# Performance work log

Hardware: AMD Instinct MI355X
Metric: run time of the kernel (lower is better)

## Reference

```python
import jax, jax.numpy as jnp
import numpy as np

MODEL_DIM = 1024
TOTAL_DIM = 1024
N_HEADS = 16
HEAD_DIM = TOTAL_DIM // N_HEADS


def setup_inputs() -> dict:
    key = jax.random.key(0)
    k1, k2, k3 = jax.random.split(key, 3)
    query = jax.random.normal(k1, (2, 2048, MODEL_DIM), dtype=jnp.float32)
    # nn.Linear(model_dim, 3*total_dim, bias=False): store as [in, out] for x @ W
    W_in = jax.random.normal(k2, (MODEL_DIM, 3 * TOTAL_DIM), dtype=jnp.float32) / np.sqrt(MODEL_DIM)
    W_out = jax.random.normal(k3, (TOTAL_DIM, MODEL_DIM), dtype=jnp.float32) / np.sqrt(TOTAL_DIM)
    return {"query": query, "W_in": W_in, "W_out": W_out}


def reference(query, W_in, W_out):
    B, S, _ = query.shape
    qkv = query @ W_in                      # [B, S, 3*D]
    q, k, v = jnp.split(qkv, 3, axis=-1)    # each [B, S, D]

    def to_heads(t):
        return t.reshape(B, S, N_HEADS, HEAD_DIM).transpose(0, 2, 1, 3)  # [B,H,S,d]

    q, k, v = to_heads(q), to_heads(k), to_heads(v)
    scale = 1.0 / np.sqrt(HEAD_DIM).astype(np.float32)
    scores = jnp.einsum('bhqd,bhkd->bhqk', q, k) * scale  # [B,H,S,S]
    causal = jnp.tril(jnp.ones((S, S), dtype=bool))
    scores = jnp.where(causal, scores, jnp.finfo(scores.dtype).min)
    probs = jax.nn.softmax(scores, axis=-1)
    attn = jnp.einsum('bhqk,bhkd->bhqd', probs, v)        # [B,H,S,d]
    attn = attn.transpose(0, 2, 1, 3).reshape(B, S, TOTAL_DIM)
    return attn @ W_out                     # [B, S, model_dim]
```

## Files before the change

### kernel.cpp

```cpp
#include <hip/hip_runtime.h>


typedef __bf16 bf16x8 __attribute__((ext_vector_type(8)));
typedef float f32x4 __attribute__((ext_vector_type(4)));
typedef int i32x4 __attribute__((ext_vector_type(4)));

#define B_   2
#define S_   2048
#define DM   1024
#define NH   16
#define HD   64
#define N3   3072
#define M_   4096

#define SCALE_LOG2E 0.180336884f

__device__ __forceinline__ unsigned short f2bf(float f) {
  unsigned int u = __float_as_uint(f);
  u += 0x7fffu + ((u >> 16) & 1u);
  return (unsigned short)(u >> 16);
}

__device__ __forceinline__ void gload_lds16(void* lds, const void* g) {
  __builtin_amdgcn_global_load_lds(
      (__attribute__((address_space(1))) void*)g,
      (__attribute__((address_space(3))) void*)lds, 16, 0, 0);
}

__global__ __launch_bounds__(256) void f32_to_bf16_vec(
    const float4* __restrict__ in, unsigned short* __restrict__ out, int n4) {
  int i = blockIdx.x * 256 + threadIdx.x;
  if (i < n4) {
    float4 v = in[i];
    ushort4 o;
    o.x = f2bf(v.x); o.y = f2bf(v.y); o.z = f2bf(v.z); o.w = f2bf(v.w);
    *(ushort4*)(&out[(size_t)i * 4]) = o;
  }
}

__global__ __launch_bounds__(256) void transpose_f32_bf16(
    const float* __restrict__ in, unsigned short* __restrict__ out, int R, int C,
    int scale_rows, float scale) {
  __shared__ float tile[32][33];
  const int tx = threadIdx.x, ty = threadIdx.y;
  const int x = blockIdx.x * 32 + tx;
  const int y0 = blockIdx.y * 32;
#pragma unroll
  for (int j = 0; j < 32; j += 8)
    tile[ty + j][tx] = in[(size_t)(y0 + ty + j) * C + x];
  __syncthreads();
  const int ox = y0 + tx;
  const int oy0 = blockIdx.x * 32;
#pragma unroll
  for (int j = 0; j < 32; j += 8) {
    const int orow = oy0 + ty + j;
    float v = tile[tx][ty + j];
    if (orow < scale_rows) v *= scale;
    out[(size_t)orow * R + ox] = f2bf(v);
  }
}

__global__ __launch_bounds__(256) void transpose_v(
    const unsigned short* __restrict__ qkv, unsigned short* __restrict__ vT) {
  __shared__ unsigned short tile[32][33];
  const int tx = threadIdx.x, ty = threadIdx.y;
  const int c0 = blockIdx.x * 32;
  const int r0 = blockIdx.y * 32;
#pragma unroll
  for (int j = 0; j < 32; j += 8)
    tile[ty + j][tx] = qkv[(size_t)(r0 + ty + j) * N3 + 2 * DM + c0 + tx];
  __syncthreads();
  const int b = r0 >> 11;
  const int srow = (r0 & 2047);
  const int head = c0 >> 6;
#pragma unroll
  for (int j = 0; j < 32; j += 8) {
    const int d = (c0 & 63) + ty + j;
    vT[(size_t)((b * NH + head) * HD + d) * S_ + srow + tx] = tile[tx][ty + j];
  }
}

template <int OUT_BF16>
__global__ __launch_bounds__(256) void gemm_abt(
    const unsigned short* __restrict__ A, const unsigned short* __restrict__ Bt,
    void* __restrict__ Cv, int M, int N, int K) {
  __shared__ __align__(16) unsigned short a_sm[128 * 32];
  __shared__ __align__(16) unsigned short b_sm[128 * 32];
  const int tid = threadIdx.x;
  const int lane = tid & 63, wave = tid >> 6;
  const int quad = lane >> 4, l15 = lane & 15;
  const int row0 = blockIdx.y * 128, col0 = blockIdx.x * 128;
  const int wm = (wave >> 1) * 64, wn = (wave & 1) * 64;

  f32x4 acc[4][4];
#pragma unroll
  for (int i = 0; i < 4; i++)
#pragma unroll
    for (int j = 0; j < 4; j++) acc[i][j] = (f32x4){0.f, 0.f, 0.f, 0.f};

  const int e0 = tid * 8;

  for (int k0 = 0; k0 < K; k0 += 32) {
    __syncthreads();
#pragma unroll
    for (int i = 0; i < 2; i++) {
      int e = e0 + i * 2048;
      int r = e >> 5, c = e & 31;
      gload_lds16(&a_sm[e], &A[(size_t)(row0 + r) * K + k0 + c]);
      gload_lds16(&b_sm[e], &Bt[(size_t)(col0 + r) * K + k0 + c]);
    }
    __syncthreads();

    bf16x8 af[4], bfb[4];
#pragma unroll
    for (int i = 0; i < 4; i++) {
      af[i]  = *(const bf16x8*)&a_sm[(wm + i * 16 + l15) * 32 + quad * 8];
      bfb[i] = *(const bf16x8*)&b_sm[(wn + i * 16 + l15) * 32 + quad * 8];
    }
#pragma unroll
    for (int i = 0; i < 4; i++)
#pragma unroll
      for (int j = 0; j < 4; j++)
        acc[i][j] = __builtin_amdgcn_mfma_f32_16x16x32_bf16(af[i], bfb[j], acc[i][j], 0, 0, 0);
  }

#pragma unroll
  for (int i = 0; i < 4; i++) {
#pragma unroll
    for (int j = 0; j < 4; j++) {
#pragma unroll
      for (int r = 0; r < 4; r++) {
        const int row = row0 + wm + i * 16 + quad * 4 + r;
        const int col = col0 + wn + j * 16 + l15;
        const float v = acc[i][j][r];
        if (OUT_BF16)
          ((unsigned short*)Cv)[(size_t)row * N + col] = f2bf(v);
        else
          ((float*)Cv)[(size_t)row * N + col] = v;
      }
    }
  }
}

__global__ __launch_bounds__(256, 4) void attn_fused6(
    const unsigned short* __restrict__ qkv,
    const unsigned short* __restrict__ vT,
    unsigned short* __restrict__ attnout) {
  const int h = blockIdx.y, b = blockIdx.z;
  const int j = blockIdx.x;
  const int tid = threadIdx.x;
  const int lane = tid & 63, wave = tid >> 6;
  const int quad = lane >> 4, l15 = lane & 15;
  const int sw = l15 & 7;

  __shared__ __align__(16) unsigned short k_sm[2 * 4096];
  __shared__ __align__(16) unsigned short vt_sm[2 * 4096];

  const int grp = (wave < 2) ? j : (63 - j);
  const int wrow0 = grp * 32 + (wave & 1) * 16;
  const int qrow = wrow0 + l15;

  bf16x8 qf[2];
  {
    const unsigned short* qp = qkv + (size_t)(b * S_ + qrow) * N3 + h * HD + quad * 8;
    qf[0] = *(const bf16x8*)qp;
    qf[1] = *(const bf16x8*)(qp + 32);
  }

  f32x4 o[4];
#pragma unroll
  for (int n = 0; n < 4; n++) o[n] = (f32x4){0.f, 0.f, 0.f, 0.f};
  float lsum = 0.f;

  const int r0s = tid >> 3;
  const int gch = ((tid & 7) ^ (r0s & 7)) * 8;
  const unsigned short* kgb = qkv + (size_t)(b * S_ + r0s) * N3 + DM + h * HD + gch;
  const unsigned short* vgb = vT + (size_t)((b * NH + h) * HD + r0s) * S_ + gch;

  const int addrA = (((quad * 2) & 3) * 16 + l15) * 4;
  const int addrB = (((quad * 2 + 1) & 3) * 16 + l15) * 4;

  const int nt = (((63 - j) * 32 + 31) >> 6) + 1;

  gload_lds16(&k_sm[tid * 8], kgb);
  gload_lds16(&k_sm[tid * 8 + 2048], kgb + (size_t)32 * N3);
  gload_lds16(&vt_sm[tid * 8], vgb);
  gload_lds16(&vt_sm[tid * 8 + 2048], vgb + (size_t)32 * S_);

  for (int t = 0; t < nt; t++) {
    __syncthreads();
    if (t + 1 < nt) {
      const int nb = ((t + 1) & 1) * 4096;
      const unsigned short* kgt = kgb + (size_t)(t + 1) * 64 * N3;
      const unsigned short* vgt = vgb + (t + 1) * 64;
      gload_lds16(&k_sm[nb + tid * 8], kgt);
      gload_lds16(&k_sm[nb + tid * 8 + 2048], kgt + (size_t)32 * N3);
      gload_lds16(&vt_sm[nb + tid * 8], vgt);
      gload_lds16(&vt_sm[nb + tid * 8 + 2048], vgt + (size_t)32 * S_);
    }
    if (t * 64 > wrow0 + 15) continue;

    const unsigned short* kb = &k_sm[(t & 1) * 4096];
    const unsigned short* vb = &vt_sm[(t & 1) * 4096];

    f32x4 s[4];
#pragma unroll
    for (int mb = 0; mb < 4; mb++) s[mb] = (f32x4){0.f, 0.f, 0.f, 0.f};
#pragma unroll
    for (int mb = 0; mb < 4; mb++) {
      const int ro = (mb * 16 + l15) * 64;
      bf16x8 kf0 = *(const bf16x8*)&kb[ro + ((quad ^ sw) << 3)];
      bf16x8 kf1 = *(const bf16x8*)&kb[ro + (((4 + quad) ^ sw) << 3)];
      s[mb] = __builtin_amdgcn_mfma_f32_16x16x32_bf16(kf0, qf[0], s[mb], 0, 0, 0);
      s[mb] = __builtin_amdgcn_mfma_f32_16x16x32_bf16(kf1, qf[1], s[mb], 0, 0, 0);
    }

    if (t * 64 + 63 <= wrow0) {
#pragma unroll
      for (int mb = 0; mb < 4; mb++)
#pragma unroll
        for (int r = 0; r < 4; r++)
          s[mb][r] = exp2f(s[mb][r]);
    } else {
      const int kq0 = t * 64 + quad * 4;
#pragma unroll
      for (int mb = 0; mb < 4; mb++)
#pragma unroll
        for (int r = 0; r < 4; r++) {
          const float e = exp2f(s[mb][r]);
          s[mb][r] = (kq0 + mb * 16 + r <= qrow) ? e : 0.f;
        }
    }
#pragma unroll
    for (int mb = 0; mb < 4; mb++)
      lsum += (s[mb][0] + s[mb][1]) + (s[mb][2] + s[mb][3]);

    int pk[4][2];
#pragma unroll
    for (int mb = 0; mb < 4; mb++) {
      const unsigned u0 = __float_as_uint(s[mb][0]) + 0x8000u;
      const unsigned u1 = __float_as_uint(s[mb][1]) + 0x8000u;
      const unsigned u2 = __float_as_uint(s[mb][2]) + 0x8000u;
      const unsigned u3 = __float_as_uint(s[mb][3]) + 0x8000u;
      pk[mb][0] = (int)__builtin_amdgcn_perm(u1, u0, 0x07060302u);
      pk[mb][1] = (int)__builtin_amdgcn_perm(u3, u2, 0x07060302u);
    }

    const bool hi = quad >= 2;
#pragma unroll
    for (int ks = 0; ks < 2; ks++) {
      const int m0 = 2 * ks, m1 = m0 + 1;
      const int f0a = __builtin_amdgcn_ds_bpermute(addrA, pk[m0][0]);
      const int f0b = __builtin_amdgcn_ds_bpermute(addrA, pk[m1][0]);
      const int f1a = __builtin_amdgcn_ds_bpermute(addrA, pk[m0][1]);
      const int f1b = __builtin_amdgcn_ds_bpermute(addrA, pk[m1][1]);
      const int f2a = __builtin_amdgcn_ds_bpermute(addrB, pk[m0][0]);
      const int f2b = __builtin_amdgcn_ds_bpermute(addrB, pk[m1][0]);
      const int f3a = __builtin_amdgcn_ds_bpermute(addrB, pk[m0][1]);
      const int f3b = __builtin_amdgcn_ds_bpermute(addrB, pk[m1][1]);
      i32x4 fr;
      fr.x = hi ? f0b : f0a;
      fr.y = hi ? f1b : f1a;
      fr.z = hi ? f2b : f2a;
      fr.w = hi ? f3b : f3a;
      const bf16x8 pfrag = __builtin_bit_cast(bf16x8, fr);
#pragma unroll
      for (int mb = 0; mb < 4; mb++) {
        const int ro = (mb * 16 + l15) * 64;
        bf16x8 vf = *(const bf16x8*)&vb[ro + (((ks * 4 + quad) ^ sw) << 3)];
        o[mb] = __builtin_amdgcn_mfma_f32_16x16x32_bf16(vf, pfrag, o[mb], 0, 0, 0);
      }
    }
  }

  float l = lsum;
  l += __shfl_xor(l, 16);
  l += __shfl_xor(l, 32);
  const float inv = 1.0f / l;
  const size_t grow = (size_t)(b * S_ + qrow);
#pragma unroll
  for (int mb = 0; mb < 4; mb++) {
    ushort4 w;
    w.x = f2bf(o[mb][0] * inv);
    w.y = f2bf(o[mb][1] * inv);
    w.z = f2bf(o[mb][2] * inv);
    w.w = f2bf(o[mb][3] * inv);
    *(ushort4*)&attnout[grow * DM + h * HD + mb * 16 + quad * 4] = w;
  }
}

extern "C" void kernel_launch(void* const* d_in, const int* in_sizes, int n_in,
                              void* d_out, int out_size, void* d_ws, size_t ws_size,
                              hipStream_t stream) {
  const float* query = (const float*)d_in[0];
  const float* w_in  = (const float*)d_in[1];
  const float* w_out = (const float*)d_in[2];
  float* out = (float*)d_out;

  char* ws = (char*)d_ws;
  unsigned short* qbf     = (unsigned short*)(ws);
  unsigned short* vT      = (unsigned short*)(ws);
  unsigned short* w_in_t  = (unsigned short*)(ws + 8388608);
  unsigned short* w_out_t = (unsigned short*)(ws + 14680064);
  unsigned short* qkv     = (unsigned short*)(ws + 16777216);
  unsigned short* attn    = (unsigned short*)(ws + 41943040);

  f32_to_bf16_vec<<<dim3(M_ * DM / 1024), dim3(256), 0, stream>>>(
      (const float4*)query, qbf, M_ * DM / 4);
  transpose_f32_bf16<<<dim3(N3 / 32, DM / 32), dim3(32, 8), 0, stream>>>(
      w_in, w_in_t, DM, N3, DM, SCALE_LOG2E);
  transpose_f32_bf16<<<dim3(DM / 32, DM / 32), dim3(32, 8), 0, stream>>>(
      w_out, w_out_t, DM, DM, 0, 1.0f);
  gemm_abt<1><<<dim3(N3 / 128, M_ / 128), dim3(256), 0, stream>>>(qbf, w_in_t, qkv, M_, N3, DM);
  transpose_v<<<dim3(DM / 32, M_ / 32), dim3(32, 8), 0, stream>>>(qkv, vT);
  attn_fused6<<<dim3(32, NH, B_), dim3(256), 0, stream>>>(qkv, vT, attn);
  gemm_abt<0><<<dim3(DM / 128, M_ / 128), dim3(256), 0, stream>>>(attn, w_out_t, out, M_, DM, DM);
}
```

Baseline: 206.5 us.

## Rewrite attention kernel with 32x32 MFMA, split-K waves and 512-thread blocks

The attention kernel moves from 16x16x32 to 32x32x16 bf16 MFMA tiles, with each wave computing 32 query rows. Eight waves per block are paired so that each pair splits the key tiles by parity, and the partial outputs and row sums are combined through LDS at the end. Causal load balancing now comes from reversing the query-tile order for the second batch instead of pairing mirrored rows inside a block. The aim is fewer permute instructions and better MFMA efficiency, at the cost of an extra LDS reduction, higher register pressure and possibly worse balance across blocks.

```diff
diff --git a/kernel.cpp b/kernel.cpp
--- a/kernel.cpp
+++ b/kernel.cpp
@@ -3,6 +3,7 @@
 
 typedef __bf16 bf16x8 __attribute__((ext_vector_type(8)));
 typedef float f32x4 __attribute__((ext_vector_type(4)));
+typedef float f32x16 __attribute__((ext_vector_type(16)));
 typedef int i32x4 __attribute__((ext_vector_type(4)));
 
 #define B_   2
@@ -142,34 +143,35 @@
   }
 }
 
-__global__ __launch_bounds__(256, 4) void attn_fused6(
+__global__ __launch_bounds__(512, 4) void attn_fused7(
     const unsigned short* __restrict__ qkv,
     const unsigned short* __restrict__ vT,
     unsigned short* __restrict__ attnout) {
   const int h = blockIdx.y, b = blockIdx.z;
-  const int j = blockIdx.x;
+  const int qt = (b == 0) ? blockIdx.x : (15 - blockIdx.x);
   const int tid = threadIdx.x;
   const int lane = tid & 63, wave = tid >> 6;
-  const int quad = lane >> 4, l15 = lane & 15;
-  const int sw = l15 & 7;
+  const int qsub = wave >> 1, ks = wave & 1;
+  const int l31 = lane & 31, lh = lane >> 5;
+  const int swz = l31 & 7;
 
   __shared__ __align__(16) unsigned short k_sm[2 * 4096];
   __shared__ __align__(16) unsigned short vt_sm[2 * 4096];
-
-  const int grp = (wave < 2) ? j : (63 - j);
-  const int wrow0 = grp * 32 + (wave & 1) * 16;
-  const int qrow = wrow0 + l15;
-
-  bf16x8 qf[2];
+  __shared__ float lsum_sm[256];
+
+  const int qbase = qt * 128 + qsub * 32;
+  const int qrow = qbase + l31;
+
+  bf16x8 qf[4];
   {
-    const unsigned short* qp = qkv + (size_t)(b * S_ + qrow) * N3 + h * HD + quad * 8;
-    qf[0] = *(const bf16x8*)qp;
-    qf[1] = *(const bf16x8*)(qp + 32);
-  }
-
-  f32x4 o[4];
-#pragma unroll
-  for (int n = 0; n < 4; n++) o[n] = (f32x4){0.f, 0.f, 0.f, 0.f};
+    const unsigned short* qp = qkv + (size_t)(b * S_ + qrow) * N3 + h * HD + lh * 8;
+#pragma unroll
+    for (int c = 0; c < 4; c++) qf[c] = *(const bf16x8*)(qp + c * 16);
+  }
+
+  f32x16 oacc[2];
+#pragma unroll
+  for (int r = 0; r < 16; r++) { oacc[0][r] = 0.f; oacc[1][r] = 0.f; }
   float lsum = 0.f;
 
   const int r0s = tid >> 3;
@@ -177,116 +179,128 @@
   const unsigned short* kgb = qkv + (size_t)(b * S_ + r0s) * N3 + DM + h * HD + gch;
   const unsigned short* vgb = vT + (size_t)((b * NH + h) * HD + r0s) * S_ + gch;
 
-  const int addrA = (((quad * 2) & 3) * 16 + l15) * 4;
-  const int addrB = (((quad * 2 + 1) & 3) * 16 + l15) * 4;
-
-  const int nt = (((63 - j) * 32 + 31) >> 6) + 1;
-
+  const int nt = 2 * qt + 2;
   gload_lds16(&k_sm[tid * 8], kgb);
-  gload_lds16(&k_sm[tid * 8 + 2048], kgb + (size_t)32 * N3);
   gload_lds16(&vt_sm[tid * 8], vgb);
-  gload_lds16(&vt_sm[tid * 8 + 2048], vgb + (size_t)32 * S_);
 
   for (int t = 0; t < nt; t++) {
     __syncthreads();
     if (t + 1 < nt) {
       const int nb = ((t + 1) & 1) * 4096;
-      const unsigned short* kgt = kgb + (size_t)(t + 1) * 64 * N3;
-      const unsigned short* vgt = vgb + (t + 1) * 64;
-      gload_lds16(&k_sm[nb + tid * 8], kgt);
-      gload_lds16(&k_sm[nb + tid * 8 + 2048], kgt + (size_t)32 * N3);
-      gload_lds16(&vt_sm[nb + tid * 8], vgt);
-      gload_lds16(&vt_sm[nb + tid * 8 + 2048], vgt + (size_t)32 * S_);
-    }
-    if (t * 64 > wrow0 + 15) continue;
+      gload_lds16(&k_sm[nb + tid * 8], kgb + (size_t)(t + 1) * 64 * N3);
+      gload_lds16(&vt_sm[nb + tid * 8], vgb + (t + 1) * 64);
+    }
+    if (((t ^ ks) & 1) || t * 64 > qbase + 31) continue;
 
     const unsigned short* kb = &k_sm[(t & 1) * 4096];
     const unsigned short* vb = &vt_sm[(t & 1) * 4096];
 
-    f32x4 s[4];
-#pragma unroll
-    for (int mb = 0; mb < 4; mb++) s[mb] = (f32x4){0.f, 0.f, 0.f, 0.f};
-#pragma unroll
-    for (int mb = 0; mb < 4; mb++) {
-      const int ro = (mb * 16 + l15) * 64;
-      bf16x8 kf0 = *(const bf16x8*)&kb[ro + ((quad ^ sw) << 3)];
-      bf16x8 kf1 = *(const bf16x8*)&kb[ro + (((4 + quad) ^ sw) << 3)];
-      s[mb] = __builtin_amdgcn_mfma_f32_16x16x32_bf16(kf0, qf[0], s[mb], 0, 0, 0);
-      s[mb] = __builtin_amdgcn_mfma_f32_16x16x32_bf16(kf1, qf[1], s[mb], 0, 0, 0);
-    }
-
-    if (t * 64 + 63 <= wrow0) {
-#pragma unroll
-      for (int mb = 0; mb < 4; mb++)
-#pragma unroll
-        for (int r = 0; r < 4; r++)
-          s[mb][r] = exp2f(s[mb][r]);
+    f32x16 s0, s1;
+#pragma unroll
+    for (int r = 0; r < 16; r++) { s0[r] = 0.f; s1[r] = 0.f; }
+#pragma unroll
+    for (int c = 0; c < 4; c++) {
+      const int ch = ((2 * c + lh) ^ swz) * 8;
+      bf16x8 kf0 = *(const bf16x8*)&kb[l31 * 64 + ch];
+      bf16x8 kf1 = *(const bf16x8*)&kb[(32 + l31) * 64 + ch];
+      s0 = __builtin_amdgcn_mfma_f32_32x32x16_bf16(kf0, qf[c], s0, 0, 0, 0);
+      s1 = __builtin_amdgcn_mfma_f32_32x32x16_bf16(kf1, qf[c], s1, 0, 0, 0);
+    }
+
+    if (t * 64 + 63 <= qbase) {
+#pragma unroll
+      for (int r = 0; r < 16; r++) { s0[r] = exp2f(s0[r]); s1[r] = exp2f(s1[r]); }
     } else {
-      const int kq0 = t * 64 + quad * 4;
-#pragma unroll
-      for (int mb = 0; mb < 4; mb++)
-#pragma unroll
-        for (int r = 0; r < 4; r++) {
-          const float e = exp2f(s[mb][r]);
-          s[mb][r] = (kq0 + mb * 16 + r <= qrow) ? e : 0.f;
-        }
-    }
-#pragma unroll
-    for (int mb = 0; mb < 4; mb++)
-      lsum += (s[mb][0] + s[mb][1]) + (s[mb][2] + s[mb][3]);
-
-    int pk[4][2];
-#pragma unroll
-    for (int mb = 0; mb < 4; mb++) {
-      const unsigned u0 = __float_as_uint(s[mb][0]) + 0x8000u;
-      const unsigned u1 = __float_as_uint(s[mb][1]) + 0x8000u;
-      const unsigned u2 = __float_as_uint(s[mb][2]) + 0x8000u;
-      const unsigned u3 = __float_as_uint(s[mb][3]) + 0x8000u;
-      pk[mb][0] = (int)__builtin_amdgcn_perm(u1, u0, 0x07060302u);
-      pk[mb][1] = (int)__builtin_amdgcn_perm(u3, u2, 0x07060302u);
-    }
-
-    const bool hi = quad >= 2;
-#pragma unroll
-    for (int ks = 0; ks < 2; ks++) {
-      const int m0 = 2 * ks, m1 = m0 + 1;
-      const int f0a = __builtin_amdgcn_ds_bpermute(addrA, pk[m0][0]);
-      const int f0b = __builtin_amdgcn_ds_bpermute(addrA, pk[m1][0]);
-      const int f1a = __builtin_amdgcn_ds_bpermute(addrA, pk[m0][1]);
-      const int f1b = __builtin_amdgcn_ds_bpermute(addrA, pk[m1][1]);
-      const int f2a = __builtin_amdgcn_ds_bpermute(addrB, pk[m0][0]);
-      const int f2b = __builtin_amdgcn_ds_bpermute(addrB, pk[m1][0]);
-      const int f3a = __builtin_amdgcn_ds_bpermute(addrB, pk[m0][1]);
-      const int f3b = __builtin_amdgcn_ds_bpermute(addrB, pk[m1][1]);
-      i32x4 fr;
-      fr.x = hi ? f0b : f0a;
-      fr.y = hi ? f1b : f1a;
-      fr.z = hi ? f2b : f2a;
-      fr.w = hi ? f3b : f3a;
-      const bf16x8 pfrag = __builtin_bit_cast(bf16x8, fr);
-#pragma unroll
-      for (int mb = 0; mb < 4; mb++) {
-        const int ro = (mb * 16 + l15) * 64;
-        bf16x8 vf = *(const bf16x8*)&vb[ro + (((ks * 4 + quad) ^ sw) << 3)];
-        o[mb] = __builtin_amdgcn_mfma_f32_16x16x32_bf16(vf, pfrag, o[mb], 0, 0, 0);
+      const int kb4 = t * 64 + 4 * lh;
+#pragma unroll
+      for (int r = 0; r < 16; r++) {
+        const int ko = (r & 3) + 8 * (r >> 2);
+        const float e0 = exp2f(s0[r]);
+        const float e1 = exp2f(s1[r]);
+        s0[r] = (kb4 + ko <= qrow) ? e0 : 0.f;
+        s1[r] = (kb4 + 32 + ko <= qrow) ? e1 : 0.f;
       }
     }
-  }
-
-  float l = lsum;
-  l += __shfl_xor(l, 16);
-  l += __shfl_xor(l, 32);
+#pragma unroll
+    for (int r = 0; r < 16; r++) lsum += s0[r] + s1[r];
+
+#pragma unroll
+    for (int o = 0; o < 2; o++) {
+      const f32x16 sv = o ? s1 : s0;
+#pragma unroll
+      for (int c = 0; c < 2; c++) {
+        const int rb = 8 * c;
+        const unsigned u0 = __float_as_uint(sv[rb + 0]) + 0x8000u;
+        const unsigned u1 = __float_as_uint(sv[rb + 1]) + 0x8000u;
+        const unsigned u2 = __float_as_uint(sv[rb + 2]) + 0x8000u;
+        const unsigned u3 = __float_as_uint(sv[rb + 3]) + 0x8000u;
+        const unsigned u4 = __float_as_uint(sv[rb + 4]) + 0x8000u;
+        const unsigned u5 = __float_as_uint(sv[rb + 5]) + 0x8000u;
+        const unsigned u6 = __float_as_uint(sv[rb + 6]) + 0x8000u;
+        const unsigned u7 = __float_as_uint(sv[rb + 7]) + 0x8000u;
+        const int L0 = (int)__builtin_amdgcn_perm(u1, u0, 0x07060302u);
+        const int L1 = (int)__builtin_amdgcn_perm(u3, u2, 0x07060302u);
+        const int H0 = (int)__builtin_amdgcn_perm(u5, u4, 0x07060302u);
+        const int H1 = (int)__builtin_amdgcn_perm(u7, u6, 0x07060302u);
+        const int x0 = lh ? L0 : H0;
+        const int x1 = lh ? L1 : H1;
+        const int y0 = __shfl_xor(x0, 32);
+        const int y1 = __shfl_xor(x1, 32);
+        i32x4 bv;
+        bv.x = lh ? y0 : L0;
+        bv.y = lh ? y1 : L1;
+        bv.z = lh ? H0 : y0;
+        bv.w = lh ? H1 : y1;
+        const bf16x8 pfrag = __builtin_bit_cast(bf16x8, bv);
+        const int vch = ((4 * o + 2 * c + lh) ^ swz) * 8;
+        bf16x8 vf0 = *(const bf16x8*)&vb[l31 * 64 + vch];
+        bf16x8 vf1 = *(const bf16x8*)&vb[(32 + l31) * 64 + vch];
+        oacc[0] = __builtin_amdgcn_mfma_f32_32x32x16_bf16(vf0, pfrag, oacc[0], 0, 0, 0);
+        oacc[1] = __builtin_amdgcn_mfma_f32_32x32x16_bf16(vf1, pfrag, oacc[1], 0, 0, 0);
+      }
+    }
+  }
+
+  __syncthreads();
+  float* obuf = ((qsub < 2) ? (float*)k_sm : (float*)vt_sm) + (qsub & 1) * 2048;
+  if (ks == 1) {
+#pragma unroll
+    for (int od = 0; od < 2; od++)
+#pragma unroll
+      for (int g = 0; g < 4; g++) {
+        f32x4 v = {oacc[od][4 * g + 0], oacc[od][4 * g + 1],
+                   oacc[od][4 * g + 2], oacc[od][4 * g + 3]};
+        *(f32x4*)&obuf[(od * 4 + g) * 256 + lane * 4] = v;
+      }
+    lsum_sm[qsub * 64 + lane] = lsum;
+  }
+  __syncthreads();
+  if (ks == 1) return;
+
+#pragma unroll
+  for (int od = 0; od < 2; od++)
+#pragma unroll
+    for (int g = 0; g < 4; g++) {
+      const f32x4 v = *(const f32x4*)&obuf[(od * 4 + g) * 256 + lane * 4];
+#pragma unroll
+      for (int r = 0; r < 4; r++) oacc[od][4 * g + r] += v[r];
+    }
+  lsum += lsum_sm[qsub * 64 + lane];
+
+  const float l = lsum + __shfl_xor(lsum, 32);
   const float inv = 1.0f / l;
   const size_t grow = (size_t)(b * S_ + qrow);
 #pragma unroll
-  for (int mb = 0; mb < 4; mb++) {
-    ushort4 w;
-    w.x = f2bf(o[mb][0] * inv);
-    w.y = f2bf(o[mb][1] * inv);
-    w.z = f2bf(o[mb][2] * inv);
-    w.w = f2bf(o[mb][3] * inv);
-    *(ushort4*)&attnout[grow * DM + h * HD + mb * 16 + quad * 4] = w;
-  }
+  for (int od = 0; od < 2; od++)
+#pragma unroll
+    for (int g = 0; g < 4; g++) {
+      ushort4 w;
+      w.x = f2bf(oacc[od][4 * g + 0] * inv);
+      w.y = f2bf(oacc[od][4 * g + 1] * inv);
+      w.z = f2bf(oacc[od][4 * g + 2] * inv);
+      w.w = f2bf(oacc[od][4 * g + 3] * inv);
+      *(ushort4*)&attnout[grow * DM + h * HD + od * 32 + g * 8 + lh * 4] = w;
+    }
 }
 
 extern "C" void kernel_launch(void* const* d_in, const int* in_sizes, int n_in,
@@ -313,6 +327,6 @@
       w_out, w_out_t, DM, DM, 0, 1.0f);
   gemm_abt<1><<<dim3(N3 / 128, M_ / 128), dim3(256), 0, stream>>>(qbf, w_in_t, qkv, M_, N3, DM);
   transpose_v<<<dim3(DM / 32, M_ / 32), dim3(32, 8), 0, stream>>>(qkv, vT);
-  attn_fused6<<<dim3(32, NH, B_), dim3(256), 0, stream>>>(qkv, vT, attn);
+  attn_fused7<<<dim3(16, NH, B_), dim3(512), 0, stream>>>(qkv, vT, attn);
   gemm_abt<0><<<dim3(DM / 128, M_ / 128), dim3(256), 0, stream>>>(attn, w_out_t, out, M_, DM, DM);
 }
```

After: 231.3 us. 1.12x slower.

## Use 512-thread attention blocks with triple-buffered K/V and one barrier per tile

Applied to the files above, without the earlier changes.

The attention kernel now runs 8 waves per block, each block handling two 64-row query groups (one early, one late) for causal load balance, and the grid shrinks to 16 blocks per head. K and V tiles use a three-slot LDS ring so loads run two tiles ahead. Explicit vmcnt waits replace the second __syncthreads, leaving one barrier per tile. This aims to hide global latency and halve K/V traffic per query row, at the cost of more LDS per block (possibly lower occupancy) and a smaller grid.

```diff
diff --git a/kernel.cpp b/kernel.cpp
--- a/kernel.cpp
+++ b/kernel.cpp
@@ -142,7 +142,7 @@
   }
 }
 
-__global__ __launch_bounds__(256, 4) void attn_fused6(
+__global__ __launch_bounds__(512, 4) void attn_fused8(
     const unsigned short* __restrict__ qkv,
     const unsigned short* __restrict__ vT,
     unsigned short* __restrict__ attnout) {
@@ -153,11 +153,11 @@
   const int quad = lane >> 4, l15 = lane & 15;
   const int sw = l15 & 7;
 
-  __shared__ __align__(16) unsigned short k_sm[2 * 4096];
-  __shared__ __align__(16) unsigned short vt_sm[2 * 4096];
-
-  const int grp = (wave < 2) ? j : (63 - j);
-  const int wrow0 = grp * 32 + (wave & 1) * 16;
+  __shared__ __align__(16) unsigned short k_sm[3 * 4096];
+  __shared__ __align__(16) unsigned short vt_sm[3 * 4096];
+
+  const int wrow0 = (wave < 4) ? (j * 64 + wave * 16)
+                               : ((31 - j) * 64 + (wave - 4) * 16);
   const int qrow = wrow0 + l15;
 
   bf16x8 qf[2];
@@ -180,28 +180,28 @@
   const int addrA = (((quad * 2) & 3) * 16 + l15) * 4;
   const int addrB = (((quad * 2 + 1) & 3) * 16 + l15) * 4;
 
-  const int nt = (((63 - j) * 32 + 31) >> 6) + 1;
+  const int nt = 32 - j;
 
   gload_lds16(&k_sm[tid * 8], kgb);
-  gload_lds16(&k_sm[tid * 8 + 2048], kgb + (size_t)32 * N3);
   gload_lds16(&vt_sm[tid * 8], vgb);
-  gload_lds16(&vt_sm[tid * 8 + 2048], vgb + (size_t)32 * S_);
-
+  gload_lds16(&k_sm[4096 + tid * 8], kgb + (size_t)64 * N3);
+  gload_lds16(&vt_sm[4096 + tid * 8], vgb + 64);
+
+  int bt = 0;
   for (int t = 0; t < nt; t++) {
-    __syncthreads();
-    if (t + 1 < nt) {
-      const int nb = ((t + 1) & 1) * 4096;
-      const unsigned short* kgt = kgb + (size_t)(t + 1) * 64 * N3;
-      const unsigned short* vgt = vgb + (t + 1) * 64;
-      gload_lds16(&k_sm[nb + tid * 8], kgt);
-      gload_lds16(&k_sm[nb + tid * 8 + 2048], kgt + (size_t)32 * N3);
-      gload_lds16(&vt_sm[nb + tid * 8], vgt);
-      gload_lds16(&vt_sm[nb + tid * 8 + 2048], vgt + (size_t)32 * S_);
-    }
+    if (t + 1 < nt) asm volatile("s_waitcnt vmcnt(2)" ::: "memory");
+    else            asm volatile("s_waitcnt vmcnt(0)" ::: "memory");
+    __builtin_amdgcn_s_barrier();
+    __builtin_amdgcn_sched_barrier(0);
+    if (t + 2 < nt) {
+      const int b2 = (bt == 0) ? 2 : bt - 1;
+      gload_lds16(&k_sm[b2 * 4096 + tid * 8], kgb + (size_t)(t + 2) * 64 * N3);
+      gload_lds16(&vt_sm[b2 * 4096 + tid * 8], vgb + (t + 2) * 64);
+    }
+    const unsigned short* kb = &k_sm[bt * 4096];
+    const unsigned short* vb = &vt_sm[bt * 4096];
+    bt = (bt == 2) ? 0 : bt + 1;
     if (t * 64 > wrow0 + 15) continue;
-
-    const unsigned short* kb = &k_sm[(t & 1) * 4096];
-    const unsigned short* vb = &vt_sm[(t & 1) * 4096];
 
     f32x4 s[4];
 #pragma unroll
@@ -273,6 +273,8 @@
     }
   }
 
+  asm volatile("s_waitcnt vmcnt(0)" ::: "memory");
+
   float l = lsum;
   l += __shfl_xor(l, 16);
   l += __shfl_xor(l, 32);
@@ -313,6 +315,6 @@
       w_out, w_out_t, DM, DM, 0, 1.0f);
   gemm_abt<1><<<dim3(N3 / 128, M_ / 128), dim3(256), 0, stream>>>(qbf, w_in_t, qkv, M_, N3, DM);
   transpose_v<<<dim3(DM / 32, M_ / 32), dim3(32, 8), 0, stream>>>(qkv, vT);
-  attn_fused6<<<dim3(32, NH, B_), dim3(256), 0, stream>>>(qkv, vT, attn);
+  attn_fused8<<<dim3(16, NH, B_), dim3(512), 0, stream>>>(qkv, vT, attn);
   gemm_abt<0><<<dim3(DM / 128, M_ / 128), dim3(256), 0, stream>>>(attn, w_out_t, out, M_, DM, DM);
 }
```

After: 208.5 us. Within noise of the previous version (+1.0%).
